# Kernel tuning notes

Measured on AMD Instinct MI355X. Metric: run time of the kernel, lower is better.

## Reference

```python
import jax, jax.numpy as jnp
import numpy as np

H = 1024
F = 132

def _lstm_cell(x, h, c, Wih, Whh, bih, bhh):
    # PyTorch LSTMCell: gates ordered i, f, g, o
    gates = x @ Wih.T + bih + h @ Whh.T + bhh  # [B, 4H]
    i, f, g, o = jnp.split(gates, 4, axis=-1)
    i = jax.nn.sigmoid(i)
    f = jax.nn.sigmoid(f)
    g = jnp.tanh(g)
    o = jax.nn.sigmoid(o)
    c_new = f * c + i * g
    h_new = o * jnp.tanh(c_new)
    return h_new, c_new


def setup_inputs() -> dict:
    key = jax.random.key(0)
    ks = jax.random.split(key, 16)
    s = 0.02
    return {
        "initial_seq": jax.random.normal(ks[0], (32, 64, F), dtype=jnp.float32),
        "generate_frames_number": 128,
        "W_ih1": jax.random.normal(ks[1], (4 * H, F), dtype=jnp.float32) * s,
        "W_hh1": jax.random.normal(ks[2], (4 * H, H), dtype=jnp.float32) * s,
        "b_ih1": jax.random.normal(ks[3], (4 * H,), dtype=jnp.float32) * s,
        "b_hh1": jax.random.normal(ks[4], (4 * H,), dtype=jnp.float32) * s,
        "W_ih2": jax.random.normal(ks[5], (4 * H, H), dtype=jnp.float32) * s,
        "W_hh2": jax.random.normal(ks[6], (4 * H, H), dtype=jnp.float32) * s,
        "b_ih2": jax.random.normal(ks[7], (4 * H,), dtype=jnp.float32) * s,
        "b_hh2": jax.random.normal(ks[8], (4 * H,), dtype=jnp.float32) * s,
        "W_ih3": jax.random.normal(ks[9], (4 * H, H), dtype=jnp.float32) * s,
        "W_hh3": jax.random.normal(ks[10], (4 * H, H), dtype=jnp.float32) * s,
        "b_ih3": jax.random.normal(ks[11], (4 * H,), dtype=jnp.float32) * s,
        "b_hh3": jax.random.normal(ks[12], (4 * H,), dtype=jnp.float32) * s,
        "W_dec": jax.random.normal(ks[13], (F, H), dtype=jnp.float32) * s,
        "b_dec": jax.random.normal(ks[14], (F,), dtype=jnp.float32) * s,
    }


def reference(initial_seq, generate_frames_number,
              W_ih1, W_hh1, b_ih1, b_hh1,
              W_ih2, W_hh2, b_ih2, b_hh2,
              W_ih3, W_hh3, b_ih3, b_hh3,
              W_dec, b_dec):
    B = initial_seq.shape[0]
    dt = initial_seq.dtype
    zeros = jnp.zeros((B, H), dtype=dt)
    state0 = (zeros, zeros, zeros, zeros, zeros, zeros)  # h0,h1,h2,c0,c1,c2

    def step(state, in_frame):
        h0, h1, h2, c0, c1, c2 = state
        h0, c0 = _lstm_cell(in_frame, h0, c0, W_ih1, W_hh1, b_ih1, b_hh1)
        h1, c1 = _lstm_cell(h0, h1, c1, W_ih2, W_hh2, b_ih2, b_hh2)
        h2, c2 = _lstm_cell(h1, h2, c2, W_ih3, W_hh3, b_ih3, b_hh3)
        out_frame = h2 @ W_dec.T + b_dec  # [B, F]
        return (h0, h1, h2, c0, c1, c2), out_frame

    # Priming pass over the conditioning sequence (outputs discarded except last)
    def prime_step(carry, in_frame):
        state, _ = carry
        state, out = step(state, in_frame)
        return (state, out), None

    init_frame = jnp.zeros((B, F), dtype=dt)
    xs = jnp.swapaxes(initial_seq, 0, 1)  # [T, B, F]
    (state, cur_frame), _ = jax.lax.scan(prime_step, (state0, init_frame), xs)

    def gen_step(carry, _):
        state, frame = carry
        state, out = step(state, frame)
        return (state, out), out

    _, outs = jax.lax.scan(gen_step, (state, cur_frame), None,
                           length=generate_frames_number)  # [N, B, F]
    return jnp.swapaxes(outs, 0, 1)  # [B, N, F]
```

## Files before the change

kernel.cpp:

```cpp
#include <hip/hip_runtime.h>
#include <stdint.h>

typedef unsigned short u16;
typedef unsigned long long u64;
typedef __attribute__((ext_vector_type(8))) short short8;
typedef __attribute__((ext_vector_type(4))) float f32x4;

#define SZ_BIGW    (4096ull*1024ull*2ull)
#define OFF_WHH1   (0ull)
#define OFF_WIH2   (OFF_WHH1 + SZ_BIGW)
#define OFF_WHH2   (OFF_WIH2 + SZ_BIGW)
#define OFF_WIH3   (OFF_WHH2 + SZ_BIGW)
#define OFF_WHH3   (OFF_WIH3 + SZ_BIGW)
#define OFF_MCOMB  (OFF_WHH3 + SZ_BIGW)
#define OFF_WIH1   (OFF_MCOMB + SZ_BIGW)
#define SZ_WIH1    (4096ull*160ull*2ull)
#define OFF_WDECF  (OFF_WIH1 + SZ_WIH1)
#define SZ_WDECF   (160ull*1024ull*2ull)
#define OFF_WDECB  (OFF_WDECF + SZ_WDECF)
#define SZ_WDECB   (1024ull*160ull*2ull)
#define OFF_XPRIM  (OFF_WDECB + SZ_WDECB)
#define SZ_XPRIM   (64ull*5120ull*2ull)
#define OFF_H2HIST (OFF_XPRIM + SZ_XPRIM)
#define SZ_HSLOT   (32768ull*2ull)
#define SZ_H2HIST  (129ull*SZ_HSLOT)
#define OFF_H0R    (OFF_H2HIST + SZ_H2HIST)
#define SZ_HR      (192ull*SZ_HSLOT)
#define OFF_H1R    (OFF_H0R + SZ_HR)
#define OFF_H2R    (OFF_H1R + SZ_HR)
#define SZ_H2R     (64ull*SZ_HSLOT)
#define OFF_ZEROH  (OFF_H2R + SZ_H2R)
#define OFF_FLAGS  (OFF_ZEROH + SZ_HSLOT)
#define SZ_FLAGS   (4096ull)
#define OFF_BS1    (OFF_FLAGS + SZ_FLAGS)
#define OFF_BS1G   (OFF_BS1 + 16384ull)
#define OFF_BS2    (OFF_BS1G + 16384ull)
#define OFF_BS3    (OFF_BS2 + 16384ull)
#define BLOB_SIZE  (OFF_BS3 + 16384ull)

__device__ unsigned char g_blob[BLOB_SIZE];

#define ZERO_BYTES (SZ_HSLOT + SZ_FLAGS)

__device__ __forceinline__ u16 f2bf(float f) {
  unsigned u = __float_as_uint(f);
  u += 0x7fffu + ((u >> 16) & 1u);
  return (u16)(u >> 16);
}
__device__ __forceinline__ float sigm(float x) { return 1.f / (1.f + __expf(-x)); }
__device__ __forceinline__ float tanh_(float x) {
  x = fminf(fmaxf(x, -40.f), 40.f);
  float e = __expf(2.f * x);
  return (e - 1.f) / (e + 1.f);
}

__device__ __forceinline__ void dev_swizzle(const float* __restrict__ src, u16* __restrict__ dst,
                                            int J, int Jsrc, int Kpad, int Ksrc, int srcld,
                                            int transposed, int perm, int bbase, int nblocks) {
  int total = J * Kpad;
  int nkc = Kpad >> 3;
  for (int o = (blockIdx.x - bbase) * 256 + threadIdx.x; o < total; o += nblocks * 256) {
    int chunk = o >> 7, within = o & 127;
    int nt = chunk / nkc, kc = chunk - nt * nkc;
    int jr = within >> 3, ke = within & 7;
    int j = perm ? ((jr >> 2) * 1024 + nt * 4 + (jr & 3)) : (nt * 16 + jr);
    int k = kc * 8 + ke;
    float v = 0.f;
    if (j < Jsrc && k < Ksrc)
      v = transposed ? src[(size_t)k * srcld + j] : src[(size_t)j * srcld + k];
    dst[o] = f2bf(v);
  }
}

__global__ __launch_bounds__(256) void k_prep1(const float* __restrict__ s0, const float* __restrict__ s1,
                                               const float* __restrict__ s2, const float* __restrict__ s3,
                                               const float* __restrict__ s4, unsigned char* blob) {
  int m = blockIdx.x >> 9;
  const float* src = (m == 0) ? s0 : (m == 1) ? s1 : (m == 2) ? s2 : (m == 3) ? s3 : s4;
  u16* dst = (u16*)(blob + (size_t)m * SZ_BIGW);
  int nkc = 128;
  for (int o = (blockIdx.x & 511) * 256 + threadIdx.x; o < 4096 * 1024; o += 512 * 256) {
    int chunk = o >> 7, within = o & 127;
    int nt = chunk / nkc, kc = chunk - nt * nkc;
    int jr = within >> 3, ke = within & 7;
    int j = (jr >> 2) * 1024 + nt * 4 + (jr & 3);
    int k = kc * 8 + ke;
    dst[o] = f2bf(src[(size_t)j * 1024 + k]);
  }
}

__global__ __launch_bounds__(256) void k_prep2(const float* __restrict__ Wih1, const float* __restrict__ Wdec,
                                               const float* __restrict__ iseq,
                                               const float* bih1, const float* bhh1,
                                               const float* bih2, const float* bhh2,
                                               const float* bih3, const float* bhh3,
                                               const float* __restrict__ bdec, unsigned char* blob) {
  int bid = blockIdx.x;
  if (bid < 64) {
    uint4* p = (uint4*)(blob + OFF_ZEROH);
    int i = bid * 256 + threadIdx.x;
    if (i < (int)(ZERO_BYTES / 16)) p[i] = make_uint4(0u, 0u, 0u, 0u);
  } else if (bid < 320) {
    dev_swizzle(Wih1, (u16*)(blob + OFF_WIH1), 4096, 4096, 160, 132, 132, 0, 1, 64, 256);
  } else if (bid < 352) {
    dev_swizzle(Wdec, (u16*)(blob + OFF_WDECF), 160, 132, 1024, 1024, 1024, 0, 0, 320, 32);
  } else if (bid < 384) {
    dev_swizzle(Wdec, (u16*)(blob + OFF_WDECB), 1024, 1024, 160, 132, 1024, 1, 0, 352, 32);
  } else if (bid < 480) {
    u16* dst = (u16*)(blob + OFF_XPRIM);
    for (int o = (bid - 384) * 256 + threadIdx.x; o < 64 * 5120; o += 96 * 256) {
      int t = o / 5120, rem = o - t * 5120;
      int kc = rem >> 8, b = (rem >> 3) & 31, ke = rem & 7;
      int k = kc * 8 + ke;
      float v = (k < 132) ? iseq[(size_t)b * (64 * 132) + t * 132 + k] : 0.f;
      dst[o] = f2bf(v);
    }
  } else {
    int j = (bid - 480) * 256 + threadIdx.x;
    if (j < 4096) {
      float* bs1 = (float*)(blob + OFF_BS1);
      float* bs1g = (float*)(blob + OFF_BS1G);
      float* bs2 = (float*)(blob + OFF_BS2);
      float* bs3 = (float*)(blob + OFF_BS3);
      float s1 = bih1[j] + bhh1[j];
      float bc = 0.f;
      const float* wr = Wih1 + (size_t)j * 132;
      for (int f = 0; f < 132; ++f) bc += wr[f] * bdec[f];
      bs1[j] = s1;
      bs1g[j] = s1 + bc;
      bs2[j] = bih2[j] + bhh2[j];
      bs3[j] = bih3[j] + bhh3[j];
    }
  }
}

__global__ __launch_bounds__(256) void k_mcomb(const u16* __restrict__ A, const u16* __restrict__ Bm,
                                               u16* __restrict__ dst) {
  int blk = blockIdx.x;
  int mt = blk & 255, jg = blk >> 8;
  int w = threadIdx.x >> 6, l = threadIdx.x & 63, q = l >> 4, r = l & 15;
  int nt = jg * 4 + w;
  f32x4 acc = {};
  for (int ks = 0; ks < 5; ++ks) {
    short8 a = *(const short8*)(A + ((size_t)mt * 20 + ks * 4 + q) * 128 + r * 8);
    short8 b = *(const short8*)(Bm + ((size_t)nt * 20 + ks * 4 + q) * 128 + r * 8);
    acc = __builtin_amdgcn_mfma_f32_16x16x32_bf16(a, b, acc, 0, 0, 0);
  }
  int kout = nt * 16 + r;
#pragma unroll
  for (int i = 0; i < 4; ++i) {
    int jrow = q * 4 + i;
    dst[(((size_t)mt * 128 + (kout >> 3)) << 7) + jrow * 8 + (kout & 7)] = f2bf(acc[i]);
  }
}


__device__ __forceinline__ void poll3(const unsigned* p, unsigned tgt) {
  unsigned s0, s1, s2;
  asm volatile(
      "s_waitcnt vmcnt(0)\n\t"
      "global_load_dword %0, %3, off sc1\n\t"
      "global_load_dword %1, %3, off sc1\n\t"
      "global_load_dword %2, %3, off sc1\n\t"
      "WL_%=:\n\t"
      "s_waitcnt vmcnt(2)\n\t"
      "v_cmp_lt_u32 vcc, %0, %4\n\t"
      "s_cbranch_vccz WD_%=\n\t"
      "global_load_dword %0, %3, off sc1\n\t"
      "s_waitcnt vmcnt(2)\n\t"
      "v_cmp_lt_u32 vcc, %1, %4\n\t"
      "s_cbranch_vccz WD_%=\n\t"
      "global_load_dword %1, %3, off sc1\n\t"
      "s_waitcnt vmcnt(2)\n\t"
      "v_cmp_lt_u32 vcc, %2, %4\n\t"
      "s_cbranch_vccz WD_%=\n\t"
      "global_load_dword %2, %3, off sc1\n\t"
      "s_branch WL_%=\n\t"
      "WD_%=:\n\t"
      "s_waitcnt vmcnt(0)\n\t"
      : "=&v"(s0), "=&v"(s1), "=&v"(s2)
      : "v"(p), "v"(tgt)
      : "vcc", "memory");
}

__device__ __forceinline__ void wait_all(unsigned* F, unsigned tgt) {
  if (threadIdx.x < 256) poll3(F + threadIdx.x, tgt);
  __syncthreads();
}

__device__ __forceinline__ void wait_wave(unsigned* F, unsigned tgt) {
  int w = threadIdx.x >> 6, lane = threadIdx.x & 63;
  if (lane < 32) {
    unsigned p = 8u * (unsigned)w + 64u * ((unsigned)lane >> 3) + ((unsigned)lane & 7u);
    poll3(F + p, tgt);
  }
}

#define MFMA(a, b, c) __builtin_amdgcn_mfma_f32_16x16x32_bf16((a), (b), (c), 0, 0, 0)

__device__ __forceinline__ void seg_mm(f32x4& a0, f32x4& a1,
                                       const u16* __restrict__ x, const short8 (&wt)[4],
                                       int w, int q, int r) {
#pragma unroll
  for (int i = 0; i < 4; ++i) {
    const u16* xp = x + (w + 8 * i) * 1024 + q * 256 + r * 8;
    short8 t0 = *(const short8*)(xp);
    short8 t1 = *(const short8*)(xp + 128);
    a0 = MFMA(t0, wt[i], a0);
    a1 = MFMA(t1, wt[i], a1);
  }
}

template<int LBASE>
__device__ __forceinline__ void gen_phase(
    f32x4& acc0, f32x4& acc1,
    const u16* __restrict__ xa, const short8 (&wA)[4],
    unsigned* waitF, unsigned wtgt,
    const float* __restrict__ bsum, float& creg, u16* __restrict__ hout,
    unsigned* arrF, unsigned aval,
    float (*red)[2][256], int nt)
{
  int tid = threadIdx.x;
  int w = tid >> 6, l = tid & 63, q = l >> 4, r = l & 15;

  wait_wave(waitF, wtgt);

#pragma unroll
  for (int i = 0; i < 4; ++i) {
    const u16* xp = xa + (w + 8 * i) * 1024 + q * 256 + r * 8;
    short8 a0 = *(const short8*)(xp);
    short8 a1 = *(const short8*)(xp + 128);
    acc0 = MFMA(a0, wA[i], acc0);
    acc1 = MFMA(a1, wA[i], acc1);
  }

  *(f32x4*)&red[w][0][l * 4] = acc0;
  *(f32x4*)&red[w][1][l * 4] = acc1;
  __syncthreads();

  if (tid >= LBASE && tid < LBASE + 128) {
    int idx = tid - LBASE;
    int b = idx >> 2, hl = idx & 3, mt = b >> 4, row = b & 15;
    int j0 = nt * 4 + hl;
    float g4[4];
#pragma unroll
    for (int g = 0; g < 4; ++g) {
      int col = g * 4 + hl;
      int lidx = ((row >> 2) * 16 + col) * 4 + (row & 3);
      float s = bsum[g * 1024 + j0];
#pragma unroll
      for (int ww = 0; ww < 8; ++ww) s += red[ww][mt][lidx];
      g4[g] = s;
    }
    float iv = sigm(g4[0]), fv = sigm(g4[1]), gv = tanh_(g4[2]), ov = sigm(g4[3]);
    float cn = fv * creg + iv * gv;
    creg = cn;
    unsigned hv = (unsigned)f2bf(ov * tanh_(cn));
    unsigned other = __shfl_xor(hv, 1);
    if ((hl & 1) == 0) {
      unsigned packed = (hv & 0xffffu) | (other << 16);
      unsigned* dp = (unsigned*)(hout + ((size_t)(nt >> 1) * 256 +
                                         (size_t)b * 8 + (size_t)(nt & 1) * 4 + hl));
      __hip_atomic_store(dp, packed, __ATOMIC_RELAXED, __HIP_MEMORY_SCOPE_AGENT);
    }
    asm volatile("s_waitcnt vmcnt(0)" ::: "memory");
  }
  __syncthreads();

  if (tid == LBASE)
    __hip_atomic_store(arrF + nt, aval, __ATOMIC_RELAXED, __HIP_MEMORY_SCOPE_AGENT);
}

__global__ __launch_bounds__(512, 2) void k_rnn(unsigned char* blob) {
  __shared__ float red3[3][8][2][256];
  __shared__ u64 hstage[96];
  const u16* XPRIM = (const u16*)(blob + OFF_XPRIM);
  const u16* tWIH1 = (const u16*)(blob + OFF_WIH1);
  const u16* tMCOMB = (const u16*)(blob + OFF_MCOMB);
  const u16* tWHH1 = (const u16*)(blob + OFF_WHH1);
  const u16* tWIH2 = (const u16*)(blob + OFF_WIH2);
  const u16* tWHH2 = (const u16*)(blob + OFF_WHH2);
  const u16* tWIH3 = (const u16*)(blob + OFF_WIH3);
  const u16* tWHH3 = (const u16*)(blob + OFF_WHH3);
  const float* BS1 = (const float*)(blob + OFF_BS1);
  const float* BS1G = (const float*)(blob + OFF_BS1G);
  const float* BS2 = (const float*)(blob + OFF_BS2);
  const float* BS3 = (const float*)(blob + OFF_BS3);
  u16* H0R = (u16*)(blob + OFF_H0R);
  u16* H1R = (u16*)(blob + OFF_H1R);
  u16* H2R = (u16*)(blob + OFF_H2R);
  u16* H2HIST = (u16*)(blob + OFF_H2HIST);
  const u16* ZEROH = (const u16*)(blob + OFF_ZEROH);
  unsigned* FLAGS = (unsigned*)(blob + OFF_FLAGS);
  unsigned *FP = FLAGS, *F1 = FLAGS + 256, *F2 = FLAGS + 512, *F3 = FLAGS + 768;

  int nt = blockIdx.x;
  int tid = threadIdx.x;
  int w = tid >> 6, l = tid & 63, q = l >> 4, r = l & 15;
  int layer = tid >> 7, idx = tid & 127;
  const float* BSP = (layer == 0) ? BS1 : (layer == 1) ? BS2 : BS3;
  float creg = 0.f;

  short8 rWhh1[4], rWih2[4], rWhh2[4], rWih3[4], rWhh3[4];
#pragma unroll
  for (int i = 0; i < 4; ++i) {
    size_t off = (size_t)nt * 16384 + (size_t)(w + 8 * i) * 512 + (size_t)l * 8;
    rWhh1[i] = *(const short8*)(tWHH1 + off);
    rWih2[i] = *(const short8*)(tWIH2 + off);
    rWhh2[i] = *(const short8*)(tWHH2 + off);
    rWih3[i] = *(const short8*)(tWIH3 + off);
    rWhh3[i] = *(const short8*)(tWHH3 + off);
  }
  short8 rWih1 = {};
  if (w < 5)
    rWih1 = *(const short8*)(tWIH1 + (size_t)nt * 2560 + (size_t)w * 512 + (size_t)l * 8);

  for (int b = 0; b < 66; ++b) {
    f32x4 a10 = {}, a11 = {}, a20 = {}, a21 = {}, a30 = {}, a31 = {};

    if (b < 64 && w < 5) {
      const u16* xp = XPRIM + b * 5120 + w * 1024 + q * 256 + r * 8;
      short8 x0 = *(const short8*)(xp);
      short8 x1 = *(const short8*)(xp + 128);
      a10 = MFMA(x0, rWih1, a10);
      a11 = MFMA(x1, rWih1, a11);
    }

    wait_all(FP, (unsigned)b);

    if (b <= 64) {
      const u16* h0p = (b == 0) ? ZEROH : H0R + (size_t)(b - 1) * 32768;
#pragma unroll
      for (int i = 0; i < 4; ++i) {
        const u16* xp = h0p + (w + 8 * i) * 1024 + q * 256 + r * 8;
        short8 x0_ = *(const short8*)(xp);
        short8 x1_ = *(const short8*)(xp + 128);
        if (b <= 63) { a10 = MFMA(x0_, rWhh1[i], a10); a11 = MFMA(x1_, rWhh1[i], a11); }
        if (b >= 1)  { a20 = MFMA(x0_, rWih2[i], a20); a21 = MFMA(x1_, rWih2[i], a21); }
      }
    }
    if (b >= 1) {
      const u16* h1p = (b == 1) ? ZEROH : H1R + (size_t)(b - 2) * 32768;
#pragma unroll
      for (int i = 0; i < 4; ++i) {
        const u16* xp = h1p + (w + 8 * i) * 1024 + q * 256 + r * 8;
        short8 x0_ = *(const short8*)(xp);
        short8 x1_ = *(const short8*)(xp + 128);
        if (b <= 64) { a20 = MFMA(x0_, rWhh2[i], a20); a21 = MFMA(x1_, rWhh2[i], a21); }
        if (b >= 2)  { a30 = MFMA(x0_, rWih3[i], a30); a31 = MFMA(x1_, rWih3[i], a31); }
      }
    }
    if (b >= 2) {
      const u16* h2p = (b == 2) ? ZEROH : H2R + (size_t)(b - 3) * 32768;
#pragma unroll
      for (int i = 0; i < 4; ++i) {
        const u16* xp = h2p + (w + 8 * i) * 1024 + q * 256 + r * 8;
        short8 x0_ = *(const short8*)(xp);
        short8 x1_ = *(const short8*)(xp + 128);
        a30 = MFMA(x0_, rWhh3[i], a30);
        a31 = MFMA(x1_, rWhh3[i], a31);
      }
    }

    *(f32x4*)&red3[0][w][0][l * 4] = a10;  *(f32x4*)&red3[0][w][1][l * 4] = a11;
    *(f32x4*)&red3[1][w][0][l * 4] = a20;  *(f32x4*)&red3[1][w][1][l * 4] = a21;
    *(f32x4*)&red3[2][w][0][l * 4] = a30;  *(f32x4*)&red3[2][w][1][l * 4] = a31;
    __syncthreads();

    int tb = b - layer;
    if (tid < 384 && tb >= 0 && tb <= 63) {
      int bb = idx >> 2, hl = idx & 3, mt = bb >> 4, row = bb & 15;
      int j0 = nt * 4 + hl;
      float g4[4];
#pragma unroll
      for (int g = 0; g < 4; ++g) {
        int col = g * 4 + hl;
        int lidx = ((row >> 2) * 16 + col) * 4 + (row & 3);
        float s = BSP[g * 1024 + j0];
#pragma unroll
        for (int ww = 0; ww < 8; ++ww) s += red3[layer][ww][mt][lidx];
        g4[g] = s;
      }
      float iv = sigm(g4[0]), fv = sigm(g4[1]), gv = tanh_(g4[2]), ov = sigm(g4[3]);
      float cn = fv * creg + iv * gv;
      creg = cn;
      ((u16*)hstage)[tid] = f2bf(ov * tanh_(cn));
    }
    __syncthreads();

    if (tid < 64) {
      if (tid < 32) {
        size_t doff = (size_t)(nt >> 1) * 256 + (size_t)tid * 8 + (size_t)(nt & 1) * 4;
        if (b <= 63)
          __hip_atomic_store((u64*)(H0R + (size_t)b * 32768 + doff), hstage[tid],
                             __ATOMIC_RELAXED, __HIP_MEMORY_SCOPE_AGENT);
        if (b >= 1 && b <= 64)
          __hip_atomic_store((u64*)(H1R + (size_t)(b - 1) * 32768 + doff), hstage[32 + tid],
                             __ATOMIC_RELAXED, __HIP_MEMORY_SCOPE_AGENT);
        if (b >= 2) {
          u16* dst = (b < 65) ? (H2R + (size_t)(b - 2) * 32768) : H2HIST;
          __hip_atomic_store((u64*)(dst + doff), hstage[64 + tid],
                             __ATOMIC_RELAXED, __HIP_MEMORY_SCOPE_AGENT);
        }
      }
      asm volatile("s_waitcnt vmcnt(0)" ::: "memory");
      if (tid == 0)
        __hip_atomic_store(FP + nt, (unsigned)(b + 1), __ATOMIC_RELAXED, __HIP_MEMORY_SCOPE_AGENT);
    }
  }

  short8 rMcomb[4];
#pragma unroll
  for (int i = 0; i < 4; ++i)
    rMcomb[i] = *(const short8*)(tMCOMB + (size_t)nt * 16384 + (size_t)(w + 8 * i) * 512 + (size_t)l * 8);

  f32x4 c10, c11, c20, c21, c30, c31;

  c10 = {}; c11 = {};
  seg_mm(c10, c11, H0R + (size_t)63 * 32768, rWhh1, w, q, r);

  for (int t = 64; t < 192; ++t) {
    c20 = {}; c21 = {};
    seg_mm(c20, c21, H1R + (size_t)(t - 1) * 32768, rWhh2, w, q, r);

    gen_phase<0>(c10, c11, H2HIST + (size_t)(t - 64) * 32768, rMcomb,
                 (t == 64) ? FP : F3, (t == 64) ? 66u : (unsigned)(t - 64),
                 BS1G, creg, H0R + (size_t)t * 32768,
                 F1, (unsigned)(t - 63), red3[0], nt);

    c30 = {}; c31 = {};
    seg_mm(c30, c31, H2HIST + (size_t)(t - 64) * 32768, rWhh3, w, q, r);

    gen_phase<128>(c20, c21, H0R + (size_t)t * 32768, rWih2,
                   F1, (unsigned)(t - 63),
                   BS2, creg, H1R + (size_t)t * 32768,
                   F2, (unsigned)(t - 63), red3[0], nt);

    c10 = {}; c11 = {};
    if (t < 191)
      seg_mm(c10, c11, H0R + (size_t)t * 32768, rWhh1, w, q, r);

    gen_phase<256>(c30, c31, H1R + (size_t)t * 32768, rWih3,
                   F2, (unsigned)(t - 63),
                   BS3, creg, H2HIST + (size_t)(t - 63) * 32768,
                   F3, (unsigned)(t - 63), red3[0], nt);
  }
}

__global__ __launch_bounds__(256) void k_dec(const u16* __restrict__ h2hist, const u16* __restrict__ Wd,
                                             const float* __restrict__ bdec, float* __restrict__ out) {
  int blk = blockIdx.x;
  int s = blk / 10, nt = blk - s * 10;
  const u16* x = h2hist + (size_t)(s + 1) * 32768;
  int w = threadIdx.x >> 6, l = threadIdx.x & 63, q = l >> 4, r = l & 15;
  f32x4 acc[2] = {};
  for (int ks = w; ks < 32; ks += 4) {
    const u16* xp = x + ks * 1024 + q * 256 + r * 8;
    short8 a0 = *(const short8*)(xp);
    short8 a1 = *(const short8*)(xp + 128);
    short8 bf = *(const short8*)(Wd + (((size_t)nt * 128 + ks * 4) << 7) + l * 8);
    acc[0] = __builtin_amdgcn_mfma_f32_16x16x32_bf16(a0, bf, acc[0], 0, 0, 0);
    acc[1] = __builtin_amdgcn_mfma_f32_16x16x32_bf16(a1, bf, acc[1], 0, 0, 0);
  }
  __shared__ float red[4][2][256];
#pragma unroll
  for (int mt = 0; mt < 2; ++mt)
#pragma unroll
    for (int i = 0; i < 4; ++i) red[w][mt][l * 4 + i] = acc[mt][i];
  __syncthreads();
  for (int pp = threadIdx.x; pp < 512; pp += 256) {
    int b = pp >> 4, fs = pp & 15;
    int mt = b >> 4, row = b & 15;
    int lidx = ((row >> 2) * 16 + fs) * 4 + (row & 3);
    int f = nt * 16 + fs;
    if (f < 132) {
      float v = red[0][mt][lidx] + red[1][mt][lidx] + red[2][mt][lidx] + red[3][mt][lidx] + bdec[f];
      out[(size_t)b * (128 * 132) + s * 132 + f] = v;
    }
  }
}

extern "C" void kernel_launch(void* const* d_in, const int* in_sizes, int n_in,
                              void* d_out, int out_size, void* d_ws, size_t ws_size,
                              hipStream_t stream) {
  unsigned char* blob = nullptr;
  hipGetSymbolAddress((void**)&blob, HIP_SYMBOL(g_blob));

  const float* iseq = (const float*)d_in[0];
  const float* Wih1 = (const float*)d_in[2];
  const float* Whh1 = (const float*)d_in[3];
  const float* bih1 = (const float*)d_in[4];
  const float* bhh1 = (const float*)d_in[5];
  const float* Wih2 = (const float*)d_in[6];
  const float* Whh2 = (const float*)d_in[7];
  const float* bih2 = (const float*)d_in[8];
  const float* bhh2 = (const float*)d_in[9];
  const float* Wih3 = (const float*)d_in[10];
  const float* Whh3 = (const float*)d_in[11];
  const float* bih3 = (const float*)d_in[12];
  const float* bhh3 = (const float*)d_in[13];
  const float* Wdec = (const float*)d_in[14];
  const float* bdec = (const float*)d_in[15];

  u16* tWIH1 = (u16*)(blob + OFF_WIH1);
  u16* tWDECF = (u16*)(blob + OFF_WDECF);
  u16* tWDECB = (u16*)(blob + OFF_WDECB);
  u16* tMCOMB = (u16*)(blob + OFF_MCOMB);
  u16* H2HIST = (u16*)(blob + OFF_H2HIST);

  k_prep1<<<2560, 256, 0, stream>>>(Whh1, Wih2, Whh2, Wih3, Whh3, blob);
  k_prep2<<<496, 256, 0, stream>>>(Wih1, Wdec, iseq, bih1, bhh1, bih2, bhh2, bih3, bhh3, bdec, blob);
  k_mcomb<<<4096, 256, 0, stream>>>(tWIH1, tWDECB, tMCOMB);

  {
    void* args[] = { (void*)&blob };
    hipError_t ce = hipLaunchCooperativeKernel((void*)k_rnn, dim3(256), dim3(512), args, 0, stream);
    if (ce != hipSuccess) {
      k_rnn<<<dim3(256), dim3(512), 0, stream>>>(blob);
    }
  }

  k_dec<<<1280, 256, 0, stream>>>(H2HIST, tWDECF, bdec, (float*)d_out);
}
```

Measured before the change: 2.201 ms.

## Split batch across two block halves so each block syncs only with its half

Repartitions the persistent RNN grid so each block handles 16 batch rows and 8 hidden units, not 32 rows and 4 units. The batch halves become independent, so flag polling covers only the 128 blocks of the same half, which shortens the cross-block barrier. Each block now holds twice the weight registers. The combined generation matrix is streamed from global memory on every step instead of held in registers, and waves-per-EU is pinned to 2. This raises register pressure and adds global weight reads per step.

After: 2.652 ms. +20.5%, slower.

```diff
diff --git a/kernel.cpp b/kernel.cpp
--- a/kernel.cpp
+++ b/kernel.cpp
@@ -183,38 +183,40 @@
       : "vcc", "memory");
 }
 
-__device__ __forceinline__ void wait_all(unsigned* F, unsigned tgt) {
-  if (threadIdx.x < 256) poll3(F + threadIdx.x, tgt);
+__device__ __forceinline__ void wait_half(unsigned* F, unsigned tgt, int bh) {
+  if (threadIdx.x < 128) poll3(F + bh * 128 + threadIdx.x, tgt);
   __syncthreads();
 }
 
-__device__ __forceinline__ void wait_wave(unsigned* F, unsigned tgt) {
+__device__ __forceinline__ void wait_wave16(unsigned* F, unsigned tgt, int bh) {
   int w = threadIdx.x >> 6, lane = threadIdx.x & 63;
-  if (lane < 32) {
-    unsigned p = 8u * (unsigned)w + 64u * ((unsigned)lane >> 3) + ((unsigned)lane & 7u);
+  if (lane < 16) {
+    unsigned p = (unsigned)(bh * 128) + 4u * (unsigned)w + 32u * ((unsigned)lane >> 2) + ((unsigned)lane & 3u);
     poll3(F + p, tgt);
   }
 }
 
 #define MFMA(a, b, c) __builtin_amdgcn_mfma_f32_16x16x32_bf16((a), (b), (c), 0, 0, 0)
 
-__device__ __forceinline__ void seg_mm(f32x4& a0, f32x4& a1,
-                                       const u16* __restrict__ x, const short8 (&wt)[4],
-                                       int w, int q, int r) {
+__device__ __forceinline__ void seg_mmN(f32x4& a0, f32x4& a1,
+                                        const u16* __restrict__ x,
+                                        const short8 (&wa)[4], const short8 (&wb)[4],
+                                        int w, int q, int r) {
 #pragma unroll
   for (int i = 0; i < 4; ++i) {
     const u16* xp = x + (w + 8 * i) * 1024 + q * 256 + r * 8;
     short8 t0 = *(const short8*)(xp);
-    short8 t1 = *(const short8*)(xp + 128);
-    a0 = MFMA(t0, wt[i], a0);
-    a1 = MFMA(t1, wt[i], a1);
-  }
-}
-
-template<int LBASE>
+    a0 = MFMA(t0, wa[i], a0);
+    a1 = MFMA(t0, wb[i], a1);
+  }
+}
+
+template<int LBASE, int USEGB>
 __device__ __forceinline__ void gen_phase(
     f32x4& acc0, f32x4& acc1,
-    const u16* __restrict__ xa, const short8 (&wA)[4],
+    const u16* __restrict__ xa,
+    const short8 (&wAa)[4], const short8 (&wAb)[4],
+    const u16* __restrict__ gb,
     unsigned* waitF, unsigned wtgt,
     const float* __restrict__ bsum, float& creg, u16* __restrict__ hout,
     unsigned* arrF, unsigned aval,
@@ -222,16 +224,25 @@
 {
   int tid = threadIdx.x;
   int w = tid >> 6, l = tid & 63, q = l >> 4, r = l & 15;
-
-  wait_wave(waitF, wtgt);
+  int bh = nt >> 7, dt = nt & 127;
+
+  wait_wave16(waitF, wtgt, bh);
 
 #pragma unroll
   for (int i = 0; i < 4; ++i) {
-    const u16* xp = xa + (w + 8 * i) * 1024 + q * 256 + r * 8;
+    int ks = w + 8 * i;
+    const u16* xp = xa + ks * 1024 + q * 256 + r * 8;
     short8 a0 = *(const short8*)(xp);
-    short8 a1 = *(const short8*)(xp + 128);
-    acc0 = MFMA(a0, wA[i], acc0);
-    acc1 = MFMA(a1, wA[i], acc1);
+    short8 ba, bb;
+    if constexpr (USEGB) {
+      ba = *(const short8*)(gb + (size_t)ks * 512 + l * 8);
+      bb = *(const short8*)(gb + 16384 + (size_t)ks * 512 + l * 8);
+    } else {
+      ba = wAa[i];
+      bb = wAb[i];
+    }
+    acc0 = MFMA(a0, ba, acc0);
+    acc1 = MFMA(a0, bb, acc1);
   }
 
   *(f32x4*)&red[w][0][l * 4] = acc0;
@@ -240,16 +251,16 @@
 
   if (tid >= LBASE && tid < LBASE + 128) {
     int idx = tid - LBASE;
-    int b = idx >> 2, hl = idx & 3, mt = b >> 4, row = b & 15;
-    int j0 = nt * 4 + hl;
+    int b = idx >> 3, hi = idx & 7, tl = hi >> 2, hl = hi & 3;
+    int j0 = dt * 8 + hi;
     float g4[4];
 #pragma unroll
     for (int g = 0; g < 4; ++g) {
       int col = g * 4 + hl;
-      int lidx = ((row >> 2) * 16 + col) * 4 + (row & 3);
+      int lidx = ((b >> 2) * 16 + col) * 4 + (b & 3);
       float s = bsum[g * 1024 + j0];
 #pragma unroll
-      for (int ww = 0; ww < 8; ++ww) s += red[ww][mt][lidx];
+      for (int ww = 0; ww < 8; ++ww) s += red[ww][tl][lidx];
       g4[g] = s;
     }
     float iv = sigm(g4[0]), fv = sigm(g4[1]), gv = tanh_(g4[2]), ov = sigm(g4[3]);
@@ -257,11 +268,12 @@
     creg = cn;
     unsigned hv = (unsigned)f2bf(ov * tanh_(cn));
     unsigned other = __shfl_xor(hv, 1);
-    if ((hl & 1) == 0) {
+    if ((hi & 1) == 0) {
       unsigned packed = (hv & 0xffffu) | (other << 16);
-      unsigned* dp = (unsigned*)(hout + ((size_t)(nt >> 1) * 256 +
-                                         (size_t)b * 8 + (size_t)(nt & 1) * 4 + hl));
-      __hip_atomic_store(dp, packed, __ATOMIC_RELAXED, __HIP_MEMORY_SCOPE_AGENT);
+      size_t doff = (size_t)(dt >> 2) * 1024 + (size_t)(dt & 3) * 256 + (size_t)bh * 128
+                  + (size_t)b * 8 + hi;
+      __hip_atomic_store((unsigned*)(hout + doff), packed,
+                         __ATOMIC_RELAXED, __HIP_MEMORY_SCOPE_AGENT);
     }
     asm volatile("s_waitcnt vmcnt(0)" ::: "memory");
   }
@@ -271,7 +283,8 @@
     __hip_atomic_store(arrF + nt, aval, __ATOMIC_RELAXED, __HIP_MEMORY_SCOPE_AGENT);
 }
 
-__global__ __launch_bounds__(512, 2) void k_rnn(unsigned char* blob) {
+__global__ __launch_bounds__(512, 2) __attribute__((amdgpu_waves_per_eu(2, 2)))
+void k_rnn(unsigned char* blob) {
   __shared__ float red3[3][8][2][256];
   __shared__ u64 hstage[96];
   const u16* XPRIM = (const u16*)(blob + OFF_XPRIM);
@@ -295,70 +308,72 @@
   unsigned *FP = FLAGS, *F1 = FLAGS + 256, *F2 = FLAGS + 512, *F3 = FLAGS + 768;
 
   int nt = blockIdx.x;
+  int bh = nt >> 7, dt = nt & 127;
   int tid = threadIdx.x;
   int w = tid >> 6, l = tid & 63, q = l >> 4, r = l & 15;
   int layer = tid >> 7, idx = tid & 127;
   const float* BSP = (layer == 0) ? BS1 : (layer == 1) ? BS2 : BS3;
   float creg = 0.f;
 
-  short8 rWhh1[4], rWih2[4], rWhh2[4], rWih3[4], rWhh3[4];
+  short8 rWhh1a[4], rWhh1b[4], rWih2a[4], rWih2b[4], rWhh2a[4], rWhh2b[4];
+  short8 rWih3a[4], rWih3b[4], rWhh3a[4], rWhh3b[4];
 #pragma unroll
   for (int i = 0; i < 4; ++i) {
-    size_t off = (size_t)nt * 16384 + (size_t)(w + 8 * i) * 512 + (size_t)l * 8;
-    rWhh1[i] = *(const short8*)(tWHH1 + off);
-    rWih2[i] = *(const short8*)(tWIH2 + off);
-    rWhh2[i] = *(const short8*)(tWHH2 + off);
-    rWih3[i] = *(const short8*)(tWIH3 + off);
-    rWhh3[i] = *(const short8*)(tWHH3 + off);
-  }
-  short8 rWih1 = {};
-  if (w < 5)
-    rWih1 = *(const short8*)(tWIH1 + (size_t)nt * 2560 + (size_t)w * 512 + (size_t)l * 8);
+    size_t offA = (size_t)(2 * dt) * 16384 + (size_t)(w + 8 * i) * 512 + (size_t)l * 8;
+    size_t offB = offA + 16384;
+    rWhh1a[i] = *(const short8*)(tWHH1 + offA);  rWhh1b[i] = *(const short8*)(tWHH1 + offB);
+    rWih2a[i] = *(const short8*)(tWIH2 + offA);  rWih2b[i] = *(const short8*)(tWIH2 + offB);
+    rWhh2a[i] = *(const short8*)(tWHH2 + offA);  rWhh2b[i] = *(const short8*)(tWHH2 + offB);
+    rWih3a[i] = *(const short8*)(tWIH3 + offA);  rWih3b[i] = *(const short8*)(tWIH3 + offB);
+    rWhh3a[i] = *(const short8*)(tWHH3 + offA);  rWhh3b[i] = *(const short8*)(tWHH3 + offB);
+  }
+  short8 rWih1a = {}, rWih1b = {};
+  if (w < 5) {
+    size_t o1 = (size_t)(2 * dt) * 2560 + (size_t)w * 512 + (size_t)l * 8;
+    rWih1a = *(const short8*)(tWIH1 + o1);
+    rWih1b = *(const short8*)(tWIH1 + o1 + 2560);
+  }
 
   for (int b = 0; b < 66; ++b) {
     f32x4 a10 = {}, a11 = {}, a20 = {}, a21 = {}, a30 = {}, a31 = {};
 
     if (b < 64 && w < 5) {
-      const u16* xp = XPRIM + b * 5120 + w * 1024 + q * 256 + r * 8;
+      const u16* xp = XPRIM + b * 5120 + w * 1024 + q * 256 + bh * 128 + r * 8;
       short8 x0 = *(const short8*)(xp);
-      short8 x1 = *(const short8*)(xp + 128);
-      a10 = MFMA(x0, rWih1, a10);
-      a11 = MFMA(x1, rWih1, a11);
-    }
-
-    wait_all(FP, (unsigned)b);
+      a10 = MFMA(x0, rWih1a, a10);
+      a11 = MFMA(x0, rWih1b, a11);
+    }
+
+    wait_half(FP, (unsigned)b, bh);
 
     if (b <= 64) {
-      const u16* h0p = (b == 0) ? ZEROH : H0R + (size_t)(b - 1) * 32768;
+      const u16* h0p = ((b == 0) ? ZEROH : H0R + (size_t)(b - 1) * 32768) + bh * 128;
 #pragma unroll
       for (int i = 0; i < 4; ++i) {
         const u16* xp = h0p + (w + 8 * i) * 1024 + q * 256 + r * 8;
         short8 x0_ = *(const short8*)(xp);
-        short8 x1_ = *(const short8*)(xp + 128);
-        if (b <= 63) { a10 = MFMA(x0_, rWhh1[i], a10); a11 = MFMA(x1_, rWhh1[i], a11); }
-        if (b >= 1)  { a20 = MFMA(x0_, rWih2[i], a20); a21 = MFMA(x1_, rWih2[i], a21); }
+        if (b <= 63) { a10 = MFMA(x0_, rWhh1a[i], a10); a11 = MFMA(x0_, rWhh1b[i], a11); }
+        if (b >= 1)  { a20 = MFMA(x0_, rWih2a[i], a20); a21 = MFMA(x0_, rWih2b[i], a21); }
       }
     }
     if (b >= 1) {
-      const u16* h1p = (b == 1) ? ZEROH : H1R + (size_t)(b - 2) * 32768;
+      const u16* h1p = ((b == 1) ? ZEROH : H1R + (size_t)(b - 2) * 32768) + bh * 128;
 #pragma unroll
       for (int i = 0; i < 4; ++i) {
         const u16* xp = h1p + (w + 8 * i) * 1024 + q * 256 + r * 8;
         short8 x0_ = *(const short8*)(xp);
-        short8 x1_ = *(const short8*)(xp + 128);
-        if (b <= 64) { a20 = MFMA(x0_, rWhh2[i], a20); a21 = MFMA(x1_, rWhh2[i], a21); }
-        if (b >= 2)  { a30 = MFMA(x0_, rWih3[i], a30); a31 = MFMA(x1_, rWih3[i], a31); }
+        if (b <= 64) { a20 = MFMA(x0_, rWhh2a[i], a20); a21 = MFMA(x0_, rWhh2b[i], a21); }
+        if (b >= 2)  { a30 = MFMA(x0_, rWih3a[i], a30); a31 = MFMA(x0_, rWih3b[i], a31); }
       }
     }
     if (b >= 2) {
-      const u16* h2p = (b == 2) ? ZEROH : H2R + (size_t)(b - 3) * 32768;
+      const u16* h2p = ((b == 2) ? ZEROH : H2R + (size_t)(b - 3) * 32768) + bh * 128;
 #pragma unroll
       for (int i = 0; i < 4; ++i) {
         const u16* xp = h2p + (w + 8 * i) * 1024 + q * 256 + r * 8;
         short8 x0_ = *(const short8*)(xp);
-        short8 x1_ = *(const short8*)(xp + 128);
-        a30 = MFMA(x0_, rWhh3[i], a30);
-        a31 = MFMA(x1_, rWhh3[i], a31);
+        a30 = MFMA(x0_, rWhh3a[i], a30);
+        a31 = MFMA(x0_, rWhh3b[i], a31);
       }
     }
 
@@ -369,16 +384,16 @@
 
     int tb = b - layer;
     if (tid < 384 && tb >= 0 && tb <= 63) {
-      int bb = idx >> 2, hl = idx & 3, mt = bb >> 4, row = bb & 15;
-      int j0 = nt * 4 + hl;
+      int bb = idx >> 3, hi = idx & 7, tl = hi >> 2, hl = hi & 3;
+      int j0 = dt * 8 + hi;
       float g4[4];
 #pragma unroll
       for (int g = 0; g < 4; ++g) {
         int col = g * 4 + hl;
-        int lidx = ((row >> 2) * 16 + col) * 4 + (row & 3);
+        int lidx = ((bb >> 2) * 16 + col) * 4 + (bb & 3);
         float s = BSP[g * 1024 + j0];
 #pragma unroll
-        for (int ww = 0; ww < 8; ++ww) s += red3[layer][ww][mt][lidx];
+        for (int ww = 0; ww < 8; ++ww) s += red3[layer][ww][tl][lidx];
         g4[g] = s;
       }
       float iv = sigm(g4[0]), fv = sigm(g4[1]), gv = tanh_(g4[2]), ov = sigm(g4[3]);
@@ -390,7 +405,9 @@
 
     if (tid < 64) {
       if (tid < 32) {
-        size_t doff = (size_t)(nt >> 1) * 256 + (size_t)tid * 8 + (size_t)(nt & 1) * 4;
+        int bb2 = tid >> 1, hf = tid & 1;
+        size_t doff = (size_t)(dt >> 2) * 1024 + (size_t)(dt & 3) * 256 + (size_t)bh * 128
+                    + (size_t)bb2 * 8 + (size_t)hf * 4;
         if (b <= 63)
           __hip_atomic_store((u64*)(H0R + (size_t)b * 32768 + doff), hstage[tid],
                              __ATOMIC_RELAXED, __HIP_MEMORY_SCOPE_AGENT);
@@ -409,41 +426,40 @@
     }
   }
 
-  short8 rMcomb[4];
-#pragma unroll
-  for (int i = 0; i < 4; ++i)
-    rMcomb[i] = *(const short8*)(tMCOMB + (size_t)nt * 16384 + (size_t)(w + 8 * i) * 512 + (size_t)l * 8);
-
+  const u16* gbM = tMCOMB + (size_t)(2 * dt) * 16384;
   f32x4 c10, c11, c20, c21, c30, c31;
 
   c10 = {}; c11 = {};
-  seg_mm(c10, c11, H0R + (size_t)63 * 32768, rWhh1, w, q, r);
+  seg_mmN(c10, c11, H0R + (size_t)63 * 32768 + bh * 128, rWhh1a, rWhh1b, w, q, r);
 
   for (int t = 64; t < 192; ++t) {
     c20 = {}; c21 = {};
-    seg_mm(c20, c21, H1R + (size_t)(t - 1) * 32768, rWhh2, w, q, r);
-
-    gen_phase<0>(c10, c11, H2HIST + (size_t)(t - 64) * 32768, rMcomb,
-                 (t == 64) ? FP : F3, (t == 64) ? 66u : (unsigned)(t - 64),
-                 BS1G, creg, H0R + (size_t)t * 32768,
-                 F1, (unsigned)(t - 63), red3[0], nt);
+    seg_mmN(c20, c21, H1R + (size_t)(t - 1) * 32768 + bh * 128, rWhh2a, rWhh2b, w, q, r);
+
+    gen_phase<0, 1>(c10, c11, H2HIST + (size_t)(t - 64) * 32768 + bh * 128,
+                    rWhh1a, rWhh1b, gbM,
+                    (t == 64) ? FP : F3, (t == 64) ? 66u : (unsigned)(t - 64),
+                    BS1G, creg, H0R + (size_t)t * 32768,
+                    F1, (unsigned)(t - 63), red3[0], nt);
 
     c30 = {}; c31 = {};
-    seg_mm(c30, c31, H2HIST + (size_t)(t - 64) * 32768, rWhh3, w, q, r);
-
-    gen_phase<128>(c20, c21, H0R + (size_t)t * 32768, rWih2,
-                   F1, (unsigned)(t - 63),
-                   BS2, creg, H1R + (size_t)t * 32768,
-                   F2, (unsigned)(t - 63), red3[0], nt);
+    seg_mmN(c30, c31, H2HIST + (size_t)(t - 64) * 32768 + bh * 128, rWhh3a, rWhh3b, w, q, r);
+
+    gen_phase<128, 0>(c20, c21, H0R + (size_t)t * 32768 + bh * 128,
+                      rWih2a, rWih2b, nullptr,
+                      F1, (unsigned)(t - 63),
+                      BS2, creg, H1R + (size_t)t * 32768,
+                      F2, (unsigned)(t - 63), red3[0], nt);
 
     c10 = {}; c11 = {};
     if (t < 191)
-      seg_mm(c10, c11, H0R + (size_t)t * 32768, rWhh1, w, q, r);
-
-    gen_phase<256>(c30, c31, H1R + (size_t)t * 32768, rWih3,
-                   F2, (unsigned)(t - 63),
-                   BS3, creg, H2HIST + (size_t)(t - 63) * 32768,
-                   F3, (unsigned)(t - 63), red3[0], nt);
+      seg_mmN(c10, c11, H0R + (size_t)t * 32768 + bh * 128, rWhh1a, rWhh1b, w, q, r);
+
+    gen_phase<256, 0>(c30, c31, H1R + (size_t)t * 32768 + bh * 128,
+                      rWih3a, rWih3b, nullptr,
+                      F2, (unsigned)(t - 63),
+                      BS3, creg, H2HIST + (size_t)(t - 63) * 32768,
+                      F3, (unsigned)(t - 63), red3[0], nt);
   }
 }
 
```
